# Performance work log

Measured on AMD Instinct MI355X. Metric: run time of the kernel, lower is better.

## Reference

```python
import jax, jax.numpy as jnp
import numpy as np

B, F, V, D = 16384, 16, 100000, 16  # batch, n_fields, vocab, embed_dim; dims = F*D = 256
EPS = 1e-5


def _bn(x, g, b):
    # torch.nn.BatchNorm1d in training mode: biased batch variance
    m = x.mean(0)
    v = x.var(0)
    return g * (x - m) * jax.lax.rsqrt(v + EPS) + b


def setup_inputs() -> dict:
    ks = iter(jax.random.split(jax.random.key(0), 40))

    def rn(shape, s=0.05):
        return jax.random.normal(next(ks), shape, jnp.float32) * s

    return {
        "feat_ids": jax.random.randint(next(ks), (B, F), 0, V, jnp.int32),
        "domain_ids": jax.random.randint(next(ks), (B,), 0, 3, jnp.int32),
        "emb": rn((F, V, D), 0.1),
        "hW0": rn((256, 128)), "hb0": jnp.zeros(128), "hg0": jnp.ones(128), "hbe0": jnp.zeros(128),
        "hW1": rn((128, 64)), "hb1": jnp.zeros(64), "hg1": jnp.ones(64), "hbe1": jnp.zeros(64),
        "hW2": rn((64, 1024)), "hb2": jnp.zeros(1024), "hg2": jnp.ones(1024), "hbe2": jnp.zeros(1024),
        "cw": rn((3, 256)), "cb": jnp.zeros((3, 256)),
        "mW0": rn((256, 512)), "mb0": jnp.zeros(512), "mg0": jnp.ones(512), "mbe0": jnp.zeros(512),
        "mW1": rn((512, 256)), "mb1": jnp.zeros(256), "mg1": jnp.ones(256), "mbe1": jnp.zeros(256),
        "u0": rn((256, 32)), "u1": rn((32, 32)), "v0": rn((32, 32)), "v1": rn((32, 256)),
        "ab0": jnp.zeros(32), "ab1": jnp.zeros(256),
        "gamma1": jnp.ones(256), "bias1": jnp.zeros(256),
        "lw": rn((512,)), "lb": jnp.zeros(1),
    }


def _forward(feat_ids, emb, hW0, hb0, hg0, hbe0, hW1, hb1, hg1, hbe1,
             hW2, hb2, hg2, hbe2, cw, cb, mW0, mb0, mg0, mbe0,
             mW1, mb1, mg1, mbe1, u0, u1, v0, v1, ab0, ab1,
             gamma1, bias1, lw, lb):
    b, f = feat_ids.shape
    # EmbeddingLayer(squeeze_dim=True): per-field lookup then concat -> [B, F*D]
    e = emb[jnp.arange(f)[None, :], feat_ids].reshape(b, -1)
    h = e
    for W, bb, g, be in ((hW0, hb0, hg0, hbe0), (hW1, hb1, hg1, hbe1), (hW2, hb2, hg2, hbe2)):
        h = jax.nn.relu(_bn(h @ W + bb, g, be))
    k = u1.shape[0]
    H = h.reshape(b, k, k)  # [B, k, k]
    # CrossNetwork: x_{l+1} = x0 * (x_l . w_l) + b_l + x_l
    x = e
    for i in range(cw.shape[0]):
        x = e * (x @ cw[i])[:, None] + cb[i] + x
    cn_out = x  # [B, 256]
    m = e
    for W, bb, g, be in ((mW0, mb0, mg0, mbe0), (mW1, mb1, mg1, mbe1)):
        m = jax.nn.relu(_bn(m @ W + bb, g, be))
    # hyper low-rank adapter: einsum('mi,bij,jn->bmn') applied lazily so the
    # [B,256,32] per-sample weight is never materialized (associativity)
    t = jax.nn.sigmoid(jnp.einsum('bi,bij->bj', m @ u0, H) @ v0 + ab0)   # [B, 32]
    t = jnp.einsum('bi,bij->bj', t @ u1, H) @ v1 + ab1                    # [B, 256]
    mu = t.mean(0)
    var = t.var(0, ddof=1)  # torch.var default is unbiased
    m = gamma1 * (t - mu) / jnp.sqrt(var + EPS) + bias1 + m  # norm + residual
    y = jnp.concatenate([cn_out, m], axis=1) @ lw + lb[0]     # LR head
    # Every domain branch computes identical values (shared weights, full-batch
    # input, dropout p=0), so the torch.where domain-select is the identity.
    return jax.nn.sigmoid(y)  # [B]


def reference(feat_ids, domain_ids, emb, hW0, hb0, hg0, hbe0, hW1, hb1, hg1, hbe1,
              hW2, hb2, hg2, hbe2, cw, cb, mW0, mb0, mg0, mbe0,
              mW1, mb1, mg1, mbe1, u0, u1, v0, v1, ab0, ab1,
              gamma1, bias1, lw, lb):
    return _forward(feat_ids, emb, hW0, hb0, hg0, hbe0, hW1, hb1, hg1, hbe1,
                    hW2, hb2, hg2, hbe2, cw, cb, mW0, mb0, mg0, mbe0,
                    mW1, mb1, mg1, mbe1, u0, u1, v0, v1, ab0, ab1,
                    gamma1, bias1, lw, lb)
```

## Files before the change

kernel.cpp:

```cpp
#include <hip/hip_runtime.h>

typedef unsigned short u16;
typedef __attribute__((ext_vector_type(8))) short bf16x8;
typedef __attribute__((ext_vector_type(4))) float f32x4;
#define BATCH 16384

__device__ __forceinline__ float b2f(u16 u){ unsigned int i=((unsigned int)u)<<16; float f; __builtin_memcpy(&f,&i,4); return f; }
__device__ __forceinline__ u16 f2b(float f){ unsigned int x; __builtin_memcpy(&x,&f,4); unsigned int r=(x + 0x7fffu + ((x>>16)&1u))>>16; return (u16)r; }

__global__ __launch_bounds__(256) void prep_kernel(float* __restrict__ S,
                                                   const float* __restrict__ hb0, const float* __restrict__ mb0,
                                                   float* __restrict__ catb,
                                                   const float* __restrict__ w0, const float* __restrict__ w1,
                                                   const float* __restrict__ w2, const float* __restrict__ w3,
                                                   const float* __restrict__ w4, const float* __restrict__ w5,
                                                   const float* __restrict__ w6,
                                                   u16* __restrict__ catWt, u16* __restrict__ t1,
                                                   u16* __restrict__ t2, u16* __restrict__ t4,
                                                   u16* __restrict__ t5, u16* __restrict__ t6,
                                                   const int* __restrict__ ids,
                                                   const float* __restrict__ emb,
                                                   u16* __restrict__ e){
  int blk = blockIdx.x;
  int tid = threadIdx.x;
  if (blk < 18){
    int i = blk*256 + tid;
    if (i < 4480) S[i] = 0.f;
  } else if (blk == 18){
    for (int i = tid; i < 640; i += 256) catb[i] = (i < 128) ? hb0[i] : mb0[i-128];
  } else if (blk < 1523){
    int c = blk - 19;
    if (c < 640){        int idx=c*256+tid;        int n=idx>>8, k=idx&255;
                         catWt[idx] = f2b(n<128 ? w0[k*128+n] : w3[k*512+(n-128)]); }
    else if (c < 672){   int idx=(c-640)*256+tid;  t1[idx]=f2b(w1[(idx%128)*64   + idx/128]); }
    else if (c < 928){   int idx=(c-672)*256+tid;  t2[idx]=f2b(w2[(idx%64)*1024  + idx/64]);  }
    else if (c < 1440){  int idx=(c-928)*256+tid;  t4[idx]=f2b(w4[(idx%512)*256  + idx/512]); }
    else if (c < 1472){  int idx=(c-1440)*256+tid; t5[idx]=f2b(w5[(idx%256)*32   + idx/256]); }
    else {               int idx=(c-1472)*256+tid; t6[idx]=f2b(w6[(idx%32)*256   + idx/32]);  }
  } else {
    int g = blk - 1523;
    int b = g*16 + (tid >> 4), f = tid & 15;
    int id = ids[b*16 + f];
    const float4* src = (const float4*)(emb + ((size_t)f*100000 + (size_t)id)*16);
    float4 v0 = src[0], v1 = src[1], v2 = src[2], v3 = src[3];
    u16 o[16] = { f2b(v0.x),f2b(v0.y),f2b(v0.z),f2b(v0.w), f2b(v1.x),f2b(v1.y),f2b(v1.z),f2b(v1.w),
                  f2b(v2.x),f2b(v2.y),f2b(v2.z),f2b(v2.w), f2b(v3.x),f2b(v3.y),f2b(v3.z),f2b(v3.w) };
    uint4 p0, p1; __builtin_memcpy(&p0, &o[0], 16); __builtin_memcpy(&p1, &o[8], 16);
    uint4* dst = (uint4*)(e + (size_t)b*256 + f*16);
    dst[0] = p0; dst[1] = p1;
  }
}

template<int BK>
__global__ __launch_bounds__(256) void gemm_mfma(const u16* __restrict__ A,
                                                 const u16* __restrict__ Wt,
                                                 const float* __restrict__ bias,
                                                 u16* __restrict__ Ca,
                                                 u16* __restrict__ Cb,
                                                 int Nsplit,
                                                 const float* __restrict__ asums,
                                                 const float* __restrict__ asumsq,
                                                 const float* __restrict__ ag,
                                                 const float* __restrict__ abe,
                                                 float* __restrict__ sums,
                                                 float* __restrict__ sumsq,
                                                 int N, int K){
  constexpr int STR = BK + 8;
  constexpr int EPT = BK/4;
  __shared__ u16 lds[64*STR*2];
  __shared__ float bnS[512], bnB[512];
  u16* As = lds;
  u16* Bs = lds + 64*STR;
  int tid = threadIdx.x;
  int n0 = blockIdx.x*64, m0 = blockIdx.y*64;
  int lane = tid & 63, w = tid >> 6, quad = lane >> 4, m16 = lane & 15;
  int srow = tid >> 2, skoff = (tid & 3)*EPT;
  if (asums != nullptr){
    for (int k = tid; k < K; k += 256){
      float mean = asums[k] * (1.f/(float)BATCH);
      float var  = asumsq[k] * (1.f/(float)BATCH) - mean*mean;
      float sc   = ag[k] * rsqrtf(var + 1e-5f);
      bnS[k] = sc;
      bnB[k] = abe[k] - mean*sc;
    }
    __syncthreads();
  }
  f32x4 acc[4] = {};
  int ng = n0 + srow;
  uint4 a0, a1, b0, b1;
  {
    const u16* ap = A + (size_t)(m0+srow)*K + skoff;
    a0 = *(const uint4*)ap;
    if (EPT == 16) a1 = *(const uint4*)(ap + 8);
    if (ng < N){
      const u16* bp = Wt + (size_t)ng*K + skoff;
      b0 = *(const uint4*)bp;
      if (EPT == 16) b1 = *(const uint4*)(bp + 8);
    } else { b0 = make_uint4(0u,0u,0u,0u); b1 = b0; }
  }
  for (int k0 = 0; k0 < K; k0 += BK){
    u16 at[EPT];
    __builtin_memcpy(at, &a0, 16);
    if (EPT == 16) __builtin_memcpy(at+8, &a1, 16);
    if (asums != nullptr){
#pragma unroll
      for (int j=0;j<EPT;j++){
        float v = b2f(at[j]) * bnS[k0+skoff+j] + bnB[k0+skoff+j];
        at[j] = f2b(v > 0.f ? v : 0.f);
      }
    }
    uint4 s0, s1;
    __builtin_memcpy(&s0, at, 16);
    *(uint4*)&As[srow*STR + skoff] = s0;
    if (EPT == 16){ __builtin_memcpy(&s1, at+8, 16); *(uint4*)&As[srow*STR + skoff + 8] = s1; }
    *(uint4*)&Bs[srow*STR + skoff] = b0;
    if (EPT == 16) *(uint4*)&Bs[srow*STR + skoff + 8] = b1;
    if (k0 + BK < K){
      const u16* ap = A + (size_t)(m0+srow)*K + k0 + BK + skoff;
      a0 = *(const uint4*)ap;
      if (EPT == 16) a1 = *(const uint4*)(ap + 8);
      if (ng < N){
        const u16* bp = Wt + (size_t)ng*K + k0 + BK + skoff;
        b0 = *(const uint4*)bp;
        if (EPT == 16) b1 = *(const uint4*)(bp + 8);
      }
    }
    __syncthreads();
#pragma unroll
    for (int sub=0; sub<BK/32; sub++){
      bf16x8 bfrag = *(bf16x8*)&Bs[(w*16 + m16)*STR + sub*32 + quad*8];
#pragma unroll
      for (int mc=0;mc<4;mc++){
        bf16x8 afrag = *(bf16x8*)&As[(mc*16 + m16)*STR + sub*32 + quad*8];
        acc[mc] = __builtin_amdgcn_mfma_f32_16x16x32_bf16(afrag, bfrag, acc[mc], 0, 0, 0);
      }
    }
    __syncthreads();
  }
  int cw = n0 + w*16 + m16;
  float bvv = (bias != nullptr && cw < N) ? bias[cw] : 0.f;
  float cs = 0.f, cq = 0.f;
  u16* Cs = lds;
#pragma unroll
  for (int mc=0;mc<4;mc++)
#pragma unroll
    for (int r=0;r<4;r++){
      float v = acc[mc][r] + bvv;
      cs += v; cq += v*v;
      Cs[(mc*16 + quad*4 + r)*72 + w*16 + m16] = f2b(v);
    }
  if (sums != nullptr){
    cs += __shfl_xor(cs, 16, 64); cs += __shfl_xor(cs, 32, 64);
    cq += __shfl_xor(cq, 16, 64); cq += __shfl_xor(cq, 32, 64);
    if (quad == 0 && cw < N){ atomicAdd(&sums[cw], cs); atomicAdd(&sumsq[cw], cq); }
  }
  __syncthreads();
  int row = tid >> 2, c4 = (tid & 3)*16;
  int cg = n0 + c4;
  if (cg < N){
    u16* outp; int stride, colbase;
    if (Cb != nullptr && n0 >= Nsplit){ outp = Cb; stride = N - Nsplit; colbase = cg - Nsplit; }
    else if (Cb != nullptr){            outp = Ca; stride = Nsplit;     colbase = cg; }
    else {                              outp = Ca; stride = N;          colbase = cg; }
    uint4 p0 = *(uint4*)&Cs[row*72 + c4];
    uint4 p1 = *(uint4*)&Cs[row*72 + c4 + 8];
    *(uint4*)(outp + (size_t)(m0+row)*stride + colbase) = p0;
    *(uint4*)(outp + (size_t)(m0+row)*stride + colbase + 8) = p1;
  }
}

#define HSTR 1056
__global__ __launch_bounds__(512) void adapter_core(const u16* __restrict__ H,
                                                    const u16* __restrict__ Mout,
                                                    const u16* __restrict__ u0t,
                                                    const float* __restrict__ v0,
                                                    const float* __restrict__ u1,
                                                    const float* __restrict__ ab0,
                                                    const float* __restrict__ hsums,
                                                    const float* __restrict__ hsumsq,
                                                    const float* __restrict__ hg,
                                                    const float* __restrict__ hbe,
                                                    const float* __restrict__ msums,
                                                    const float* __restrict__ msumsq,
                                                    const float* __restrict__ mg,
                                                    const float* __restrict__ mbe,
                                                    u16* __restrict__ Z2){
  __shared__ __align__(16) u16 Hs[16*HSTR];
  __shared__ float bnS[1024], bnB[1024];
  __shared__ __align__(8) u16 v0s[1024], u1s[1024];
  __shared__ float mS[256], mB[256];
  __shared__ __align__(16) u16 aS[16*256];
  __shared__ float Ps[512], qs[512], t1s[512], ss[512];
  __shared__ float ab0s[32];
  int tid = threadIdx.x;
  int r = tid >> 5, j = tid & 31;
  size_t row0 = (size_t)blockIdx.x * 16;

  for (int k = tid; k < 1024; k += 512){
    float mean = hsums[k] * (1.f/(float)BATCH);
    float var  = hsumsq[k] * (1.f/(float)BATCH) - mean*mean;
    float sc   = hg[k] * rsqrtf(var + 1e-5f);
    bnS[k] = sc; bnB[k] = hbe[k] - mean*sc;
  }
  if (tid < 256){
    float4 a = *(const float4*)(v0 + tid*4);
    ushort4 pa = { f2b(a.x), f2b(a.y), f2b(a.z), f2b(a.w) };
    *(ushort4*)&v0s[tid*4] = pa;
    float4 b4 = *(const float4*)(u1 + tid*4);
    ushort4 pb = { f2b(b4.x), f2b(b4.y), f2b(b4.z), f2b(b4.w) };
    *(ushort4*)&u1s[tid*4] = pb;
  } else {
    int c = tid - 256;
    float mean = msums[c] * (1.f/(float)BATCH);
    float var  = msumsq[c] * (1.f/(float)BATCH) - mean*mean;
    float sc   = mg[c] * rsqrtf(var + 1e-5f);
    mS[c] = sc; mB[c] = mbe[c] - mean*sc;
  }
  if (tid < 32) ab0s[tid] = ab0[tid];
  __syncthreads();

  {
    int el = tid*8;
    int col = el & 255;
    uint4 mv = *(const uint4*)(Mout + row0*256 + el);
    u16 mt[8]; __builtin_memcpy(mt, &mv, 16);
#pragma unroll
    for (int q=0;q<8;q++){
      float v = b2f(mt[q]) * mS[col+q] + mB[col+q];
      mt[q] = f2b(v > 0.f ? v : 0.f);
    }
    uint4 so; __builtin_memcpy(&so, mt, 16);
    *(uint4*)&aS[el] = so;
  }
#pragma unroll
  for (int it=0; it<4; it++){
    int el = it*4096 + tid*8;
    int rr = el >> 10, col = el & 1023;
    uint4 hv = *(const uint4*)(H + row0*1024 + el);
    u16 ht[8]; __builtin_memcpy(ht, &hv, 16);
#pragma unroll
    for (int q=0;q<8;q++){
      float v = b2f(ht[q]) * bnS[col+q] + bnB[col+q];
      ht[q] = f2b(v > 0.f ? v : 0.f);
    }
    uint4 so; __builtin_memcpy(&so, ht, 16);
    *(uint4*)&Hs[rr*HSTR + col] = so;
  }
  __syncthreads();

  {
    float acc = 0.f;
    for (int k8 = 0; k8 < 256; k8 += 8){
      uint4 vu = *(const uint4*)(u0t + j*256 + k8);
      uint4 va; __builtin_memcpy(&va, &aS[r*256 + k8], 16);
      u16 ta[8], tu[8]; __builtin_memcpy(ta, &va, 16); __builtin_memcpy(tu, &vu, 16);
#pragma unroll
      for (int q=0;q<8;q++) acc += b2f(ta[q]) * b2f(tu[q]);
    }
    Ps[tid] = acc;
  }
  __syncthreads();

  float acc = 0.f;
#pragma unroll
  for (int i=0;i<32;i++) acc += Ps[r*32+i] * b2f(Hs[r*HSTR + i*32 + j]);
  qs[tid] = acc;
  __syncthreads();
  acc = ab0s[j];
#pragma unroll
  for (int i=0;i<32;i++) acc += qs[r*32+i] * b2f(v0s[i*32+j]);
  t1s[tid] = 1.f / (1.f + __expf(-acc));
  __syncthreads();
  acc = 0.f;
#pragma unroll
  for (int i=0;i<32;i++) acc += t1s[r*32+i] * b2f(u1s[i*32+j]);
  ss[tid] = acc;
  __syncthreads();
  acc = 0.f;
#pragma unroll
  for (int i=0;i<32;i++) acc += ss[r*32+i] * b2f(Hs[r*HSTR + i*32 + j]);
  Z2[(row0 + r)*32 + j] = f2b(acc);
}

__global__ __launch_bounds__(256) void final_kernel(const u16* __restrict__ e,
                                                    const float* __restrict__ cw,
                                                    const float* __restrict__ cb,
                                                    const u16* __restrict__ t,
                                                    const u16* __restrict__ mo,
                                                    const float* __restrict__ tsums,
                                                    const float* __restrict__ tsumsq,
                                                    const float* __restrict__ tg,
                                                    const float* __restrict__ tbe,
                                                    const float* __restrict__ msums,
                                                    const float* __restrict__ msumsq,
                                                    const float* __restrict__ mg,
                                                    const float* __restrict__ mbe,
                                                    const float* __restrict__ lw,
                                                    const float* __restrict__ lb,
                                                    float* __restrict__ out){
  __shared__ float tS[256], tB[256], mS[256], mB[256];
  int tid = threadIdx.x;
  {
    int c = tid;
    float mean = tsums[c] * (1.f/(float)BATCH);
    float var  = (tsumsq[c] - mean*mean*(float)BATCH) * (1.f/(float)(BATCH-1));
    float sc   = tg[c] * rsqrtf(var + 1e-5f);
    tS[c] = sc; tB[c] = tbe[c] - mean*sc;
    float mmean = msums[c] * (1.f/(float)BATCH);
    float mvar  = msumsq[c] * (1.f/(float)BATCH) - mmean*mmean;
    float msc   = mg[c] * rsqrtf(mvar + 1e-5f);
    mS[c] = msc; mB[c] = mbe[c] - mmean*msc;
  }
  __syncthreads();
  int wave = tid >> 6, lane = tid & 63;
  int b = blockIdx.x*4 + wave;
  int n4 = lane*4;
  ushort4 ev = *(const ushort4*)(e + (size_t)b*256 + n4);
  float ec[4] = { b2f(ev.x), b2f(ev.y), b2f(ev.z), b2f(ev.w) };
  float x[4]  = { ec[0], ec[1], ec[2], ec[3] };
  for (int i=0;i<3;i++){
    float p = 0.f;
#pragma unroll
    for (int q=0;q<4;q++) p += x[q] * cw[i*256 + n4 + q];
#pragma unroll
    for (int o=1;o<64;o<<=1) p += __shfl_xor(p, o, 64);
#pragma unroll
    for (int q=0;q<4;q++) x[q] = ec[q]*p + cb[i*256 + n4 + q] + x[q];
  }
  ushort4 tv = *(const ushort4*)(t  + (size_t)b*256 + n4);
  ushort4 mv = *(const ushort4*)(mo + (size_t)b*256 + n4);
  float ta[4] = { b2f(tv.x), b2f(tv.y), b2f(tv.z), b2f(tv.w) };
  float ma[4] = { b2f(mv.x), b2f(mv.y), b2f(mv.z), b2f(mv.w) };
  float p = 0.f;
#pragma unroll
  for (int q=0;q<4;q++){
    int n = n4 + q;
    p += x[q] * lw[n];
    float mr = ma[q]*mS[n] + mB[n];
    mr = mr > 0.f ? mr : 0.f;
    float mf = tS[n]*ta[q] + tB[n] + mr;
    p += mf * lw[256 + n];
  }
#pragma unroll
  for (int o=32;o>0;o>>=1) p += __shfl_down(p, o, 64);
  if (lane == 0){
    float y = p + lb[0];
    out[b] = 1.f / (1.f + __expf(-y));
  }
}

extern "C" void kernel_launch(void* const* d_in, const int* in_sizes, int n_in,
                              void* d_out, int out_size, void* d_ws, size_t ws_size,
                              hipStream_t stream) {
  const int B = BATCH;
  const int*   feat = (const int*)d_in[0];
  const float* emb  = (const float*)d_in[2];
  const float* hW0 = (const float*)d_in[3],  *hb0 = (const float*)d_in[4],  *hg0 = (const float*)d_in[5],  *hbe0 = (const float*)d_in[6];
  const float* hW1 = (const float*)d_in[7],  *hb1 = (const float*)d_in[8],  *hg1 = (const float*)d_in[9],  *hbe1 = (const float*)d_in[10];
  const float* hW2 = (const float*)d_in[11], *hb2 = (const float*)d_in[12], *hg2 = (const float*)d_in[13], *hbe2 = (const float*)d_in[14];
  const float* cw  = (const float*)d_in[15], *cb  = (const float*)d_in[16];
  const float* mW0 = (const float*)d_in[17], *mb0 = (const float*)d_in[18], *mg0 = (const float*)d_in[19], *mbe0 = (const float*)d_in[20];
  const float* mW1 = (const float*)d_in[21], *mb1 = (const float*)d_in[22], *mg1 = (const float*)d_in[23], *mbe1 = (const float*)d_in[24];
  const float* u0  = (const float*)d_in[25], *u1  = (const float*)d_in[26];
  const float* v0  = (const float*)d_in[27], *v1  = (const float*)d_in[28];
  const float* ab0 = (const float*)d_in[29], *ab1 = (const float*)d_in[30];
  const float* gamma1 = (const float*)d_in[31], *bias1 = (const float*)d_in[32];
  const float* lw  = (const float*)d_in[33], *lb = (const float*)d_in[34];
  float* out = (float*)d_out;

  char* base = (char*)d_ws;
  const size_t MB = 1024*1024;
  u16* H    = (u16*)(base);
  u16* e    = (u16*)(base + 32*MB);
  u16* Y0   = (u16*)(base + 40*MB);
  u16* Y1   = (u16*)(base + 44*MB);
  u16* M0   = (u16*)(base + 48*MB);
  u16* Mout = (u16*)(base + 64*MB);
  u16* T    = (u16*)(base + 72*MB);
  u16* Z2   = (u16*)(base + 80*MB);
  u16* catWt= (u16*)(base + 88*MB);
  u16* hW1t = catWt + 163840;
  u16* hW2t = hW1t + 8192;
  u16* mW1t = hW2t + 65536;
  u16* u0t  = mW1t + 131072;
  u16* v1t  = u0t + 8192;
  float* catb = (float*)(v1t + 8192);
  float* S    = catb + 640;

  prep_kernel<<<2547, 256, 0, stream>>>(S, hb0, mb0, catb,
                                        hW0, hW1, hW2, mW0, mW1, u0, v1,
                                        catWt, hW1t, hW2t, mW1t, u0t, v1t,
                                        feat, emb, e);

  gemm_mfma<64><<<dim3(10, B/64), 256, 0, stream>>>(e, catWt, catb, Y0, M0, 128,
      nullptr, nullptr, nullptr, nullptr, S+0, S+640, 640, 256);

  gemm_mfma<64><<<dim3(1, B/64), 256, 0, stream>>>(Y0, hW1t, hb1, Y1, nullptr, 0,
      S+0, S+640, hg0, hbe0, S+1280, S+1344, 64, 128);
  gemm_mfma<64><<<dim3(16, B/64), 256, 0, stream>>>(Y1, hW2t, hb2, H, nullptr, 0,
      S+1280, S+1344, hg1, hbe1, S+1408, S+2432, 1024, 64);

  gemm_mfma<64><<<dim3(4, B/64), 256, 0, stream>>>(M0, mW1t, mb1, Mout, nullptr, 0,
      S+128, S+768, mg0, mbe0, S+3456, S+3712, 256, 512);

  adapter_core<<<B/16, 512, 0, stream>>>(H, Mout, u0t, v0, u1, ab0,
      S+1408, S+2432, hg2, hbe2, S+3456, S+3712, mg1, mbe1, Z2);
  gemm_mfma<32><<<dim3(4, B/64), 256, 0, stream>>>(Z2, v1t, ab1, T, nullptr, 0,
      nullptr, nullptr, nullptr, nullptr, S+3968, S+4224, 256, 32);

  final_kernel<<<B/4, 256, 0, stream>>>(e, cw, cb, T, Mout,
      S+3968, S+4224, gamma1, bias1,
      S+3456, S+3712, mg1, mbe1, lw, lb, out);
}
```

Measured before the change: 326.7 us.

## Derive hyper-net layer-3 BN stats from Gram matrix and recompute H in adapter

```diff
diff --git a/kernel.cpp b/kernel.cpp
--- a/kernel.cpp
+++ b/kernel.cpp
@@ -23,13 +23,13 @@
                                                    u16* __restrict__ e){
   int blk = blockIdx.x;
   int tid = threadIdx.x;
-  if (blk < 18){
+  if (blk < 34){
     int i = blk*256 + tid;
-    if (i < 4480) S[i] = 0.f;
-  } else if (blk == 18){
+    if (i < 8640) S[i] = 0.f;
+  } else if (blk == 34){
     for (int i = tid; i < 640; i += 256) catb[i] = (i < 128) ? hb0[i] : mb0[i-128];
-  } else if (blk < 1523){
-    int c = blk - 19;
+  } else if (blk < 1539){
+    int c = blk - 35;
     if (c < 640){        int idx=c*256+tid;        int n=idx>>8, k=idx&255;
                          catWt[idx] = f2b(n<128 ? w0[k*128+n] : w3[k*512+(n-128)]); }
     else if (c < 672){   int idx=(c-640)*256+tid;  t1[idx]=f2b(w1[(idx%128)*64   + idx/128]); }
@@ -38,7 +38,7 @@
     else if (c < 1472){  int idx=(c-1440)*256+tid; t5[idx]=f2b(w5[(idx%256)*32   + idx/256]); }
     else {               int idx=(c-1472)*256+tid; t6[idx]=f2b(w6[(idx%32)*256   + idx/32]);  }
   } else {
-    int g = blk - 1523;
+    int g = blk - 1539;
     int b = g*16 + (tid >> 4), f = tid & 15;
     int id = ids[b*16 + f];
     const float4* src = (const float4*)(emb + ((size_t)f*100000 + (size_t)id)*16);
@@ -169,10 +169,104 @@
   }
 }
 
+__global__ __launch_bounds__(256) void gram_kernel(const u16* __restrict__ Y1,
+                                                   const float* __restrict__ ysums,
+                                                   const float* __restrict__ ysumsq,
+                                                   const float* __restrict__ yg,
+                                                   const float* __restrict__ ybe,
+                                                   u16* __restrict__ Y1p,
+                                                   float* __restrict__ gsum,
+                                                   float* __restrict__ G){
+  __shared__ u16 As[64*72];
+  __shared__ float bnSy[64], bnBy[64];
+  int tid = threadIdx.x;
+  int row0 = blockIdx.x*64;
+  if (tid < 64){
+    float mean = ysums[tid] * (1.f/(float)BATCH);
+    float var  = ysumsq[tid] * (1.f/(float)BATCH) - mean*mean;
+    float sc   = yg[tid] * rsqrtf(var + 1e-5f);
+    bnSy[tid] = sc; bnBy[tid] = ybe[tid] - mean*sc;
+  }
+  __syncthreads();
+  {
+    int r = tid >> 2, c0 = (tid & 3)*16;
+    const u16* src = Y1 + (size_t)(row0 + r)*64 + c0;
+    uint4 v0 = *(const uint4*)src;
+    uint4 v1 = *(const uint4*)(src + 8);
+    u16 t[16]; __builtin_memcpy(t, &v0, 16); __builtin_memcpy(t+8, &v1, 16);
+#pragma unroll
+    for (int q=0;q<16;q++){
+      float v = b2f(t[q]) * bnSy[c0+q] + bnBy[c0+q];
+      t[q] = f2b(v > 0.f ? v : 0.f);
+    }
+    uint4 s0, s1; __builtin_memcpy(&s0, t, 16); __builtin_memcpy(&s1, t+8, 16);
+    *(uint4*)&As[r*72 + c0] = s0;
+    *(uint4*)&As[r*72 + c0 + 8] = s1;
+    u16* dst = Y1p + (size_t)(row0 + r)*64 + c0;
+    *(uint4*)dst = s0;
+    *(uint4*)(dst + 8) = s1;
+  }
+  __syncthreads();
+  if (tid < 64){
+    float s = 0.f;
+    for (int r = 0; r < 64; r++) s += b2f(As[r*72 + tid]);
+    atomicAdd(&gsum[tid], s);
+  }
+  {
+    int i = tid >> 2, j0 = (tid & 3)*16;
+    float acc[16] = {};
+    for (int r = 0; r < 64; r++){
+      float ai = b2f(As[r*72 + i]);
+#pragma unroll
+      for (int jj=0;jj<16;jj++) acc[jj] += ai * b2f(As[r*72 + j0 + jj]);
+    }
+#pragma unroll
+    for (int jj=0;jj<16;jj++) atomicAdd(&G[i*64 + j0 + jj], acc[jj]);
+  }
+}
+
+__global__ __launch_bounds__(256) void hstats_kernel(const float* __restrict__ gsum,
+                                                     const float* __restrict__ G,
+                                                     const u16* __restrict__ hW2t,
+                                                     const float* __restrict__ hb2,
+                                                     float* __restrict__ hsums,
+                                                     float* __restrict__ hsumsq){
+  __shared__ float Gs[4096];
+  __shared__ float gs[64];
+  int tid = threadIdx.x;
+  for (int k = tid; k < 4096; k += 256) Gs[k] = G[k];
+  if (tid < 64) gs[tid] = gsum[tid];
+  __syncthreads();
+  int c = blockIdx.x*256 + tid;
+  float w[64];
+#pragma unroll
+  for (int k8 = 0; k8 < 64; k8 += 8){
+    uint4 v = *(const uint4*)(hW2t + (size_t)c*64 + k8);
+    u16 t[8]; __builtin_memcpy(t, &v, 16);
+#pragma unroll
+    for (int q=0;q<8;q++) w[k8+q] = b2f(t[q]);
+  }
+  float s1 = 0.f;
+#pragma unroll
+  for (int k=0;k<64;k++) s1 += gs[k]*w[k];
+  float q = 0.f;
+  for (int i=0;i<64;i++){
+    float t = 0.f;
+#pragma unroll
+    for (int j=0;j<64;j++) t += Gs[i*64+j]*w[j];
+    q += w[i]*t;
+  }
+  float beta = hb2[c];
+  hsums[c]  = s1 + (float)BATCH*beta;
+  hsumsq[c] = q + 2.f*beta*s1 + (float)BATCH*beta*beta;
+}
+
 #define HSTR 1056
-__global__ __launch_bounds__(512) void adapter_core(const u16* __restrict__ H,
+__global__ __launch_bounds__(512) void adapter_core(const u16* __restrict__ Y1p,
                                                     const u16* __restrict__ Mout,
                                                     const u16* __restrict__ u0t,
+                                                    const u16* __restrict__ hW2t,
+                                                    const float* __restrict__ hb2,
                                                     const float* __restrict__ v0,
                                                     const float* __restrict__ u1,
                                                     const float* __restrict__ ab0,
@@ -186,7 +280,8 @@
                                                     const float* __restrict__ mbe,
                                                     u16* __restrict__ Z2){
   __shared__ __align__(16) u16 Hs[16*HSTR];
-  __shared__ float bnS[1024], bnB[1024];
+  __shared__ __align__(16) u16 Y1s[16*72];
+  __shared__ float bnS[1024], bnB2[1024];
   __shared__ __align__(8) u16 v0s[1024], u1s[1024];
   __shared__ float mS[256], mB[256];
   __shared__ __align__(16) u16 aS[16*256];
@@ -194,13 +289,14 @@
   __shared__ float ab0s[32];
   int tid = threadIdx.x;
   int r = tid >> 5, j = tid & 31;
+  int lane = tid & 63, wv = tid >> 6, quad = lane >> 4, m16 = lane & 15;
   size_t row0 = (size_t)blockIdx.x * 16;
 
   for (int k = tid; k < 1024; k += 512){
     float mean = hsums[k] * (1.f/(float)BATCH);
     float var  = hsumsq[k] * (1.f/(float)BATCH) - mean*mean;
     float sc   = hg[k] * rsqrtf(var + 1e-5f);
-    bnS[k] = sc; bnB[k] = hbe[k] - mean*sc;
+    bnS[k] = sc; bnB2[k] = hbe[k] - mean*sc + sc*hb2[k];
   }
   if (tid < 256){
     float4 a = *(const float4*)(v0 + tid*4);
@@ -216,14 +312,22 @@
     float sc   = mg[c] * rsqrtf(var + 1e-5f);
     mS[c] = sc; mB[c] = mbe[c] - mean*sc;
   }
+  if (tid < 128){
+    int el = tid*8, rr = el >> 6, col = el & 63;
+    uint4 v = *(const uint4*)(Y1p + row0*64 + el);
+    *(uint4*)&Y1s[rr*72 + col] = v;
+  }
+  {
+    int el = tid*8;
+    uint4 mv = *(const uint4*)(Mout + row0*256 + el);
+    *(uint4*)&aS[el] = mv;
+  }
   if (tid < 32) ab0s[tid] = ab0[tid];
   __syncthreads();
 
   {
-    int el = tid*8;
-    int col = el & 255;
-    uint4 mv = *(const uint4*)(Mout + row0*256 + el);
-    u16 mt[8]; __builtin_memcpy(mt, &mv, 16);
+    int el = tid*8, col = el & 255;
+    u16 mt[8]; __builtin_memcpy(mt, &aS[el], 16);
 #pragma unroll
     for (int q=0;q<8;q++){
       float v = b2f(mt[q]) * mS[col+q] + mB[col+q];
@@ -232,19 +336,26 @@
     uint4 so; __builtin_memcpy(&so, mt, 16);
     *(uint4*)&aS[el] = so;
   }
-#pragma unroll
-  for (int it=0; it<4; it++){
-    int el = it*4096 + tid*8;
-    int rr = el >> 10, col = el & 1023;
-    uint4 hv = *(const uint4*)(H + row0*1024 + el);
-    u16 ht[8]; __builtin_memcpy(ht, &hv, 16);
-#pragma unroll
-    for (int q=0;q<8;q++){
-      float v = b2f(ht[q]) * bnS[col+q] + bnB[col+q];
-      ht[q] = f2b(v > 0.f ? v : 0.f);
-    }
-    uint4 so; __builtin_memcpy(&so, ht, 16);
-    *(uint4*)&Hs[rr*HSTR + col] = so;
+  {
+    bf16x8 af0 = *(bf16x8*)&Y1s[m16*72 + quad*8];
+    bf16x8 af1 = *(bf16x8*)&Y1s[m16*72 + 32 + quad*8];
+#pragma unroll
+    for (int i=0;i<8;i++){
+      int nt = wv*8 + i;
+      const u16* bp = hW2t + (size_t)(nt*16 + m16)*64;
+      bf16x8 bf0 = *(bf16x8*)(bp + quad*8);
+      bf16x8 bf1 = *(bf16x8*)(bp + 32 + quad*8);
+      f32x4 acc = {};
+      acc = __builtin_amdgcn_mfma_f32_16x16x32_bf16(af0, bf0, acc, 0, 0, 0);
+      acc = __builtin_amdgcn_mfma_f32_16x16x32_bf16(af1, bf1, acc, 0, 0, 0);
+      int c = nt*16 + m16;
+      float s = bnS[c], b = bnB2[c];
+#pragma unroll
+      for (int rr=0;rr<4;rr++){
+        float v = acc[rr]*s + b;
+        Hs[(quad*4+rr)*HSTR + c] = f2b(v > 0.f ? v : 0.f);
+      }
+    }
   }
   __syncthreads();
 
@@ -370,7 +481,7 @@
 
   char* base = (char*)d_ws;
   const size_t MB = 1024*1024;
-  u16* H    = (u16*)(base);
+  u16* Y1p  = (u16*)(base);
   u16* e    = (u16*)(base + 32*MB);
   u16* Y0   = (u16*)(base + 40*MB);
   u16* Y1   = (u16*)(base + 44*MB);
@@ -386,8 +497,10 @@
   u16* v1t  = u0t + 8192;
   float* catb = (float*)(v1t + 8192);
   float* S    = catb + 640;
-
-  prep_kernel<<<2547, 256, 0, stream>>>(S, hb0, mb0, catb,
+  float* gsum = S + 4480;
+  float* G    = S + 4544;
+
+  prep_kernel<<<2563, 256, 0, stream>>>(S, hb0, mb0, catb,
                                         hW0, hW1, hW2, mW0, mW1, u0, v1,
                                         catWt, hW1t, hW2t, mW1t, u0t, v1t,
                                         feat, emb, e);
@@ -397,13 +510,13 @@
 
   gemm_mfma<64><<<dim3(1, B/64), 256, 0, stream>>>(Y0, hW1t, hb1, Y1, nullptr, 0,
       S+0, S+640, hg0, hbe0, S+1280, S+1344, 64, 128);
-  gemm_mfma<64><<<dim3(16, B/64), 256, 0, stream>>>(Y1, hW2t, hb2, H, nullptr, 0,
-      S+1280, S+1344, hg1, hbe1, S+1408, S+2432, 1024, 64);
+  gram_kernel<<<256, 256, 0, stream>>>(Y1, S+1280, S+1344, hg1, hbe1, Y1p, gsum, G);
+  hstats_kernel<<<4, 256, 0, stream>>>(gsum, G, hW2t, hb2, S+1408, S+2432);
 
   gemm_mfma<64><<<dim3(4, B/64), 256, 0, stream>>>(M0, mW1t, mb1, Mout, nullptr, 0,
       S+128, S+768, mg0, mbe0, S+3456, S+3712, 256, 512);
 
-  adapter_core<<<B/16, 512, 0, stream>>>(H, Mout, u0t, v0, u1, ab0,
+  adapter_core<<<B/16, 512, 0, stream>>>(Y1p, Mout, u0t, hW2t, hb2, v0, u1, ab0,
       S+1408, S+2432, hg2, hbe2, S+3456, S+3712, mg1, mbe1, Z2);
   gemm_mfma<32><<<dim3(4, B/64), 256, 0, stream>>>(Z2, v1t, ab1, T, nullptr, 0,
       nullptr, nullptr, nullptr, nullptr, S+3968, S+4224, 256, 32);
```

After: 559.5 us. 1.71x slower.

## Merge two independent GEMMs into one launch and shrink adapter LDS footprint

Applied to the files above, without the earlier changes.

```diff
diff --git a/kernel.cpp b/kernel.cpp
--- a/kernel.cpp
+++ b/kernel.cpp
@@ -52,27 +52,25 @@
 }
 
 template<int BK>
-__global__ __launch_bounds__(256) void gemm_mfma(const u16* __restrict__ A,
-                                                 const u16* __restrict__ Wt,
-                                                 const float* __restrict__ bias,
-                                                 u16* __restrict__ Ca,
-                                                 u16* __restrict__ Cb,
-                                                 int Nsplit,
-                                                 const float* __restrict__ asums,
-                                                 const float* __restrict__ asumsq,
-                                                 const float* __restrict__ ag,
-                                                 const float* __restrict__ abe,
-                                                 float* __restrict__ sums,
-                                                 float* __restrict__ sumsq,
-                                                 int N, int K){
+__device__ __forceinline__ void gemm_body(const u16* __restrict__ A,
+                                          const u16* __restrict__ Wt,
+                                          const float* __restrict__ bias,
+                                          u16* __restrict__ Ca,
+                                          u16* __restrict__ Cb,
+                                          int Nsplit,
+                                          const float* __restrict__ asums,
+                                          const float* __restrict__ asumsq,
+                                          const float* __restrict__ ag,
+                                          const float* __restrict__ abe,
+                                          float* __restrict__ sums,
+                                          float* __restrict__ sumsq,
+                                          int N, int K, int n0, int m0,
+                                          u16* lds, float* bnS, float* bnB){
   constexpr int STR = BK + 8;
   constexpr int EPT = BK/4;
-  __shared__ u16 lds[64*STR*2];
-  __shared__ float bnS[512], bnB[512];
   u16* As = lds;
   u16* Bs = lds + 64*STR;
   int tid = threadIdx.x;
-  int n0 = blockIdx.x*64, m0 = blockIdx.y*64;
   int lane = tid & 63, w = tid >> 6, quad = lane >> 4, m16 = lane & 15;
   int srow = tid >> 2, skoff = (tid & 3)*EPT;
   if (asums != nullptr){
@@ -166,6 +164,54 @@
     uint4 p1 = *(uint4*)&Cs[row*72 + c4 + 8];
     *(uint4*)(outp + (size_t)(m0+row)*stride + colbase) = p0;
     *(uint4*)(outp + (size_t)(m0+row)*stride + colbase + 8) = p1;
+  }
+}
+
+template<int BK>
+__global__ __launch_bounds__(256) void gemm_mfma(const u16* __restrict__ A,
+                                                 const u16* __restrict__ Wt,
+                                                 const float* __restrict__ bias,
+                                                 u16* __restrict__ Ca,
+                                                 u16* __restrict__ Cb,
+                                                 int Nsplit,
+                                                 const float* __restrict__ asums,
+                                                 const float* __restrict__ asumsq,
+                                                 const float* __restrict__ ag,
+                                                 const float* __restrict__ abe,
+                                                 float* __restrict__ sums,
+                                                 float* __restrict__ sumsq,
+                                                 int N, int K){
+  constexpr int STR = BK + 8;
+  __shared__ u16 lds[64*STR*2];
+  __shared__ float bnS[512], bnB[512];
+  gemm_body<BK>(A, Wt, bias, Ca, Cb, Nsplit, asums, asumsq, ag, abe,
+                sums, sumsq, N, K, blockIdx.x*64, blockIdx.y*64, lds, bnS, bnB);
+}
+
+__global__ __launch_bounds__(256) void gemm_dual(
+    const u16* __restrict__ A1, const u16* __restrict__ Wt1, const float* __restrict__ b1,
+    u16* __restrict__ C1,
+    const float* __restrict__ as1, const float* __restrict__ aq1,
+    const float* __restrict__ g1v, const float* __restrict__ be1,
+    float* __restrict__ s1, float* __restrict__ q1, int N1, int K1, int nb1, int nblk1,
+    const u16* __restrict__ A2, const u16* __restrict__ Wt2, const float* __restrict__ b2,
+    u16* __restrict__ C2,
+    const float* __restrict__ as2, const float* __restrict__ aq2,
+    const float* __restrict__ g2v, const float* __restrict__ be2,
+    float* __restrict__ s2, float* __restrict__ q2, int N2, int K2, int nblk2){
+  constexpr int STR = 64 + 8;
+  __shared__ u16 lds[64*STR*2];
+  __shared__ float bnS[512], bnB[512];
+  int blk = blockIdx.x;
+  if (blk < nb1){
+    int n0 = (blk % nblk1)*64, m0 = (blk / nblk1)*64;
+    gemm_body<64>(A1, Wt1, b1, C1, nullptr, 0, as1, aq1, g1v, be1,
+                  s1, q1, N1, K1, n0, m0, lds, bnS, bnB);
+  } else {
+    int q = blk - nb1;
+    int n0 = (q % nblk2)*64, m0 = (q / nblk2)*64;
+    gemm_body<64>(A2, Wt2, b2, C2, nullptr, 0, as2, aq2, g2v, be2,
+                  s2, q2, N2, K2, n0, m0, lds, bnS, bnB);
   }
 }
 
@@ -189,12 +235,12 @@
   __shared__ float bnS[1024], bnB[1024];
   __shared__ __align__(8) u16 v0s[1024], u1s[1024];
   __shared__ float mS[256], mB[256];
-  __shared__ __align__(16) u16 aS[16*256];
-  __shared__ float Ps[512], qs[512], t1s[512], ss[512];
+  __shared__ float PT[512], QS[512];
   __shared__ float ab0s[32];
   int tid = threadIdx.x;
   int r = tid >> 5, j = tid & 31;
   size_t row0 = (size_t)blockIdx.x * 16;
+  u16* aS = Hs;
 
   for (int k = tid; k < 1024; k += 512){
     float mean = hsums[k] * (1.f/(float)BATCH);
@@ -216,14 +262,17 @@
     float sc   = mg[c] * rsqrtf(var + 1e-5f);
     mS[c] = sc; mB[c] = mbe[c] - mean*sc;
   }
-  if (tid < 32) ab0s[tid] = ab0[tid];
-  __syncthreads();
-
   {
     int el = tid*8;
-    int col = el & 255;
     uint4 mv = *(const uint4*)(Mout + row0*256 + el);
-    u16 mt[8]; __builtin_memcpy(mt, &mv, 16);
+    *(uint4*)&aS[el] = mv;
+  }
+  if (tid < 32) ab0s[tid] = ab0[tid];
+  __syncthreads();
+
+  {
+    int el = tid*8, col = el & 255;
+    u16 mt[8]; __builtin_memcpy(mt, &aS[el], 16);
 #pragma unroll
     for (int q=0;q<8;q++){
       float v = b2f(mt[q]) * mS[col+q] + mB[col+q];
@@ -231,20 +280,6 @@
     }
     uint4 so; __builtin_memcpy(&so, mt, 16);
     *(uint4*)&aS[el] = so;
-  }
-#pragma unroll
-  for (int it=0; it<4; it++){
-    int el = it*4096 + tid*8;
-    int rr = el >> 10, col = el & 1023;
-    uint4 hv = *(const uint4*)(H + row0*1024 + el);
-    u16 ht[8]; __builtin_memcpy(ht, &hv, 16);
-#pragma unroll
-    for (int q=0;q<8;q++){
-      float v = b2f(ht[q]) * bnS[col+q] + bnB[col+q];
-      ht[q] = f2b(v > 0.f ? v : 0.f);
-    }
-    uint4 so; __builtin_memcpy(&so, ht, 16);
-    *(uint4*)&Hs[rr*HSTR + col] = so;
   }
   __syncthreads();
 
@@ -257,28 +292,44 @@
 #pragma unroll
       for (int q=0;q<8;q++) acc += b2f(ta[q]) * b2f(tu[q]);
     }
-    Ps[tid] = acc;
+    PT[tid] = acc;
+  }
+  __syncthreads();
+
+#pragma unroll
+  for (int it=0; it<4; it++){
+    int el = it*4096 + tid*8;
+    int rr = el >> 10, col = el & 1023;
+    uint4 hv = *(const uint4*)(H + row0*1024 + el);
+    u16 ht[8]; __builtin_memcpy(ht, &hv, 16);
+#pragma unroll
+    for (int q=0;q<8;q++){
+      float v = b2f(ht[q]) * bnS[col+q] + bnB[col+q];
+      ht[q] = f2b(v > 0.f ? v : 0.f);
+    }
+    uint4 so; __builtin_memcpy(&so, ht, 16);
+    *(uint4*)&Hs[rr*HSTR + col] = so;
   }
   __syncthreads();
 
   float acc = 0.f;
 #pragma unroll
-  for (int i=0;i<32;i++) acc += Ps[r*32+i] * b2f(Hs[r*HSTR + i*32 + j]);
-  qs[tid] = acc;
+  for (int i=0;i<32;i++) acc += PT[r*32+i] * b2f(Hs[r*HSTR + i*32 + j]);
+  QS[tid] = acc;
   __syncthreads();
   acc = ab0s[j];
 #pragma unroll
-  for (int i=0;i<32;i++) acc += qs[r*32+i] * b2f(v0s[i*32+j]);
-  t1s[tid] = 1.f / (1.f + __expf(-acc));
+  for (int i=0;i<32;i++) acc += QS[r*32+i] * b2f(v0s[i*32+j]);
+  PT[tid] = 1.f / (1.f + __expf(-acc));
   __syncthreads();
   acc = 0.f;
 #pragma unroll
-  for (int i=0;i<32;i++) acc += t1s[r*32+i] * b2f(u1s[i*32+j]);
-  ss[tid] = acc;
+  for (int i=0;i<32;i++) acc += PT[r*32+i] * b2f(u1s[i*32+j]);
+  QS[tid] = acc;
   __syncthreads();
   acc = 0.f;
 #pragma unroll
-  for (int i=0;i<32;i++) acc += ss[r*32+i] * b2f(Hs[r*HSTR + i*32 + j]);
+  for (int i=0;i<32;i++) acc += QS[r*32+i] * b2f(Hs[r*HSTR + i*32 + j]);
   Z2[(row0 + r)*32 + j] = f2b(acc);
 }
 
@@ -395,13 +446,12 @@
   gemm_mfma<64><<<dim3(10, B/64), 256, 0, stream>>>(e, catWt, catb, Y0, M0, 128,
       nullptr, nullptr, nullptr, nullptr, S+0, S+640, 640, 256);
 
-  gemm_mfma<64><<<dim3(1, B/64), 256, 0, stream>>>(Y0, hW1t, hb1, Y1, nullptr, 0,
-      S+0, S+640, hg0, hbe0, S+1280, S+1344, 64, 128);
+  gemm_dual<<<1280, 256, 0, stream>>>(
+      Y0, hW1t, hb1, Y1, S+0, S+640, hg0, hbe0, S+1280, S+1344, 64, 128, 256, 1,
+      M0, mW1t, mb1, Mout, S+128, S+768, mg0, mbe0, S+3456, S+3712, 256, 512, 4);
+
   gemm_mfma<64><<<dim3(16, B/64), 256, 0, stream>>>(Y1, hW2t, hb2, H, nullptr, 0,
       S+1280, S+1344, hg1, hbe1, S+1408, S+2432, 1024, 64);
-
-  gemm_mfma<64><<<dim3(4, B/64), 256, 0, stream>>>(M0, mW1t, mb1, Mout, nullptr, 0,
-      S+128, S+768, mg0, mbe0, S+3456, S+3712, 256, 512);
 
   adapter_core<<<B/16, 512, 0, stream>>>(H, Mout, u0t, v0, u1, ab0,
       S+1408, S+2432, hg2, hbe2, S+3456, S+3712, mg1, mbe1, Z2);
```

New measurement: 323.5 us. About the same (-1.0%).
